# Kernel tuning notes

Hardware: AMD Instinct MI355X
Metric: run time of the kernel (lower is better)

## Reference

```python
import jax, jax.numpy as jnp
import numpy as np

SIZE = 2
STRIDE = 1


def _odd_shapes(input_size, k, size, stride):
    # Mirrors maxpool2d.shape_for_odd_columns. slices=[row_start,row_end,col_start,col_end]
    slices = [None, None, None, None]
    pads = [0, 0, 0, 0]  # (left, right, top, bottom) -- torch ZeroPad2d order
    pads[0] = k
    pads[1] = max(0, k - (input_size[3] - 1) % (2 * stride))
    pads[2] = size - k // 2
    constraint = input_size[2] - 1 - ((input_size[2] - 1 - stride // 2) // stride) * stride
    bottom = size - (k + 1) // 2 - constraint
    if bottom >= 0:
        pads[3] = bottom
    else:
        slices[1] = bottom
    return slices, pads


def _even_shapes(input_size, k, size, stride):
    # Mirrors maxpool2d.shape_for_even_columns
    slices = [None, None, None, None]
    pads = [0, 0, 0, 0]
    left = k - stride
    if left >= 0:
        pads[0] = left
    else:
        slices[2] = -left
    pads[1] = max(0, k - (input_size[3] - 1 - stride) % (2 * stride))
    top_shift = -(k % 2) if stride % 2 == 1 else 0
    top = size - k // 2 + top_shift - stride // 2
    if top >= 0:
        pads[2] = top
    else:
        slices[0] = -top
    bottom_shift = 0 if stride % 2 == 1 else -(k % 2)
    pads[3] = max(0, size - k // 2 + bottom_shift - (input_size[2] - stride // 2 - 1) % stride)
    return slices, pads


def _max_pool2d(x, kernel, stride, dilation):
    # Equivalent of F.max_pool2d with VALID padding + window dilation.
    init = jnp.array(-jnp.inf, x.dtype)
    return jax.lax.reduce_window(
        x, init, jax.lax.max,
        window_dimensions=(1, 1, kernel[0], kernel[1]),
        window_strides=(1, 1, stride[0], stride[1]),
        padding='VALID',
        window_dilation=(1, 1, dilation[0], dilation[1]),
    )


def _branch(x, slices, pads, kernel, stride, dilation):
    s0, s1, s2, s3 = slices
    x = x[:, :, s0:s1, s2:s3]
    # torch ZeroPad2d pads with zeros (data values), so zeros participate in max.
    x = jnp.pad(x, ((0, 0), (0, 0), (pads[2], pads[3]), (pads[0], pads[1])))
    return _max_pool2d(x, kernel, stride, dilation)


def _hex_maxpool(x, size, stride):
    input_size = x.shape  # (B, C, H, W) -- all static under jit
    odd = None
    even = None
    for i in range(size + 1):
        kernel = (1 + 2 * size - i, 1 if i == 0 else 2)
        dilation = (1, 1) if i == 0 else (1, 2 * i)
        pool_stride = (stride, 2 * stride)
        o_sl, o_pd = _odd_shapes(input_size, i, size, stride)
        e_sl, e_pd = _even_shapes(input_size, i, size, stride)
        o = _branch(x, o_sl, o_pd, kernel, pool_stride, dilation)
        e = _branch(x, e_sl, e_pd, kernel, pool_stride, dilation)
        odd = o if odd is None else jnp.maximum(odd, o)
        even = e if even is None else jnp.maximum(even, e)
    cat = jnp.concatenate((odd, even), axis=3)
    n_odd = odd.shape[3]
    n_even = even.shape[3]
    if n_odd == n_even:
        idx = [i + x_ * n_even for i in range(n_even) for x_ in range(2)]
    else:
        idx = [i + x_ * n_odd for i in range(n_even) for x_ in range(2)]
        idx.append(n_even)
    return cat[:, :, :, np.asarray(idx)]


def setup_inputs() -> dict:
    key = jax.random.key(0)
    x = jax.random.normal(key, (16, 64, 256, 256), dtype=jnp.float32)
    return {"input": x}


def reference(input) -> jnp.ndarray:
    return _hex_maxpool(input, SIZE, STRIDE)
```

## Files before the change

kernel.cpp:

```cpp
#include <hip/hip_runtime.h>

#define IMG_H 256
#define IMG_W 256
#define ROWS_PER_WAVE 64
#define STRIPS 4
#define N_IMG 1024

__device__ __forceinline__ float4 fmax4(const float4 a, const float4 b) {
    return make_float4(fmaxf(a.x, b.x), fmaxf(a.y, b.y), fmaxf(a.z, b.z), fmaxf(a.w, b.w));
}

__global__ __launch_bounds__(256) void hex_maxpool_kernel(const float* __restrict__ in,
                                                          float* __restrict__ out) {
    const int lane  = threadIdx.x & 63;
    const int wave  = threadIdx.x >> 6;
    const int gw    = blockIdx.x * 4 + wave;
    const int img   = gw >> 2;
    const int strip = gw & 3;
    const int h0    = strip * ROWS_PER_WAVE;
    const int col   = lane * 4;

    const float* p = in  + (size_t)img * (IMG_H * IMG_W);
    float*       q = out + (size_t)img * (IMG_H * IMG_W);

    auto load_row = [&](int r) -> float4 {
        if ((unsigned)r < (unsigned)IMG_H) {
            return *reinterpret_cast<const float4*>(p + r * IMG_W + col);
        }
        return make_float4(0.f, 0.f, 0.f, 0.f);
    };

    float4 w0 = load_row(h0 - 2);
    float4 w1 = load_row(h0 - 1);
    float4 w2 = load_row(h0);
    float4 w3 = load_row(h0 + 1);
    float4 w4 = load_row(h0 + 2);

    for (int h = h0; h < h0 + ROWS_PER_WAVE; ++h) {
        const float4 wn = load_row(h + 3);

        const float4 m3 = fmax4(fmax4(w1, w2), w3);
        const float4 bu = fmax4(m3, w0);
        const float4 bd = fmax4(m3, w4);
        const float4 a5 = fmax4(bu, w4);

        float Lbuw = __shfl_up(bu.w, 1);
        float Lm3z = __shfl_up(m3.z, 1);
        float Lm3w = __shfl_up(m3.w, 1);
        float Rbdx = __shfl_down(bd.x, 1);
        float Rm3x = __shfl_down(m3.x, 1);
        float Rm3y = __shfl_down(m3.y, 1);
        if (lane == 0)  { Lbuw = 0.f; Lm3z = 0.f; Lm3w = 0.f; }
        if (lane == 63) { Rbdx = 0.f; Rm3x = 0.f; Rm3y = 0.f; }

        float4 o;
        o.x = fmaxf(fmaxf(fmaxf(a5.x, Lbuw), bu.y), fmaxf(Lm3z, m3.z));
        o.y = fmaxf(fmaxf(fmaxf(a5.y, bd.x), bd.z), fmaxf(Lm3w, m3.w));
        o.z = fmaxf(fmaxf(fmaxf(a5.z, bu.y), bu.w), fmaxf(m3.x, Rm3x));
        o.w = fmaxf(fmaxf(fmaxf(a5.w, bd.z), Rbdx), fmaxf(m3.y, Rm3y));

        *reinterpret_cast<float4*>(q + h * IMG_W + col) = o;

        w0 = w1; w1 = w2; w2 = w3; w3 = w4; w4 = wn;
    }
}

extern "C" void kernel_launch(void* const* d_in, const int* in_sizes, int n_in,
                              void* d_out, int out_size, void* d_ws, size_t ws_size,
                              hipStream_t stream) {
    (void)in_sizes; (void)n_in; (void)d_ws; (void)ws_size; (void)out_size;
    const float* in = (const float*)d_in[0];
    float* out = (float*)d_out;
    hex_maxpool_kernel<<<N_IMG * STRIPS / 4, 256, 0, stream>>>(in, out);
}
```

Before: 437.6 us.

## Split images into 16-row strips staged through LDS via direct global-to-LDS loads

```diff
diff --git a/kernel.cpp b/kernel.cpp
--- a/kernel.cpp
+++ b/kernel.cpp
@@ -1,9 +1,11 @@
 #include <hip/hip_runtime.h>
+#include <stdint.h>
 
 #define IMG_H 256
 #define IMG_W 256
-#define ROWS_PER_WAVE 64
-#define STRIPS 4
+#define STRIP_ROWS 16
+#define LDS_ROWS   20
+#define STRIPS_PER_IMG 16
 #define N_IMG 1024
 
 __device__ __forceinline__ float4 fmax4(const float4 a, const float4 b) {
@@ -12,33 +14,36 @@
 
 __global__ __launch_bounds__(256) void hex_maxpool_kernel(const float* __restrict__ in,
                                                           float* __restrict__ out) {
+    __shared__ float smem[LDS_ROWS * IMG_W];
+
     const int lane  = threadIdx.x & 63;
     const int wave  = threadIdx.x >> 6;
-    const int gw    = blockIdx.x * 4 + wave;
-    const int img   = gw >> 2;
-    const int strip = gw & 3;
-    const int h0    = strip * ROWS_PER_WAVE;
-    const int col   = lane * 4;
+    const int img   = blockIdx.x >> 4;
+    const int strip = blockIdx.x & 15;
+    const int S     = strip * STRIP_ROWS;
 
     const float* p = in  + (size_t)img * (IMG_H * IMG_W);
     float*       q = out + (size_t)img * (IMG_H * IMG_W);
 
-    auto load_row = [&](int r) -> float4 {
-        if ((unsigned)r < (unsigned)IMG_H) {
-            return *reinterpret_cast<const float4*>(p + r * IMG_W + col);
+#pragma unroll
+    for (int j5 = 0; j5 < 5; ++j5) {
+        const int j = wave * 5 + j5;
+        const int g = S - 2 + j;
+        if ((unsigned)g < (unsigned)IMG_H) {
+            const float* gp = p + (size_t)g * IMG_W + lane * 4;
+            __builtin_amdgcn_global_load_lds(
+                (const __attribute__((address_space(1))) uint32_t*)gp,
+                (__attribute__((address_space(3))) uint32_t*)&smem[j * IMG_W],
+                16, 0, 0);
+        } else {
+            *reinterpret_cast<float4*>(&smem[j * IMG_W + lane * 4]) =
+                make_float4(0.f, 0.f, 0.f, 0.f);
         }
-        return make_float4(0.f, 0.f, 0.f, 0.f);
-    };
+    }
+    __syncthreads();
 
-    float4 w0 = load_row(h0 - 2);
-    float4 w1 = load_row(h0 - 1);
-    float4 w2 = load_row(h0);
-    float4 w3 = load_row(h0 + 1);
-    float4 w4 = load_row(h0 + 2);
-
-    for (int h = h0; h < h0 + ROWS_PER_WAVE; ++h) {
-        const float4 wn = load_row(h + 3);
-
+    auto hexrow = [&](const float4 w0, const float4 w1, const float4 w2,
+                      const float4 w3, const float4 w4) -> float4 {
         const float4 m3 = fmax4(fmax4(w1, w2), w3);
         const float4 bu = fmax4(m3, w0);
         const float4 bd = fmax4(m3, w4);
@@ -58,10 +63,20 @@
         o.y = fmaxf(fmaxf(fmaxf(a5.y, bd.x), bd.z), fmaxf(Lm3w, m3.w));
         o.z = fmaxf(fmaxf(fmaxf(a5.z, bu.y), bu.w), fmaxf(m3.x, Rm3x));
         o.w = fmaxf(fmaxf(fmaxf(a5.w, bd.z), Rbdx), fmaxf(m3.y, Rm3y));
+        return o;
+    };
 
-        *reinterpret_cast<float4*>(q + h * IMG_W + col) = o;
+    const int base = wave * 4;
+    float4 r[8];
+#pragma unroll
+    for (int j = 0; j < 8; ++j) {
+        r[j] = *reinterpret_cast<const float4*>(&smem[(base + j) * IMG_W + lane * 4]);
+    }
 
-        w0 = w1; w1 = w2; w2 = w3; w3 = w4; w4 = wn;
+#pragma unroll
+    for (int k = 0; k < 4; ++k) {
+        const float4 o = hexrow(r[k], r[k + 1], r[k + 2], r[k + 3], r[k + 4]);
+        *reinterpret_cast<float4*>(q + (size_t)(S + base + k) * IMG_W + lane * 4) = o;
     }
 }
 
@@ -71,5 +86,5 @@
     (void)in_sizes; (void)n_in; (void)d_ws; (void)ws_size; (void)out_size;
     const float* in = (const float*)d_in[0];
     float* out = (float*)d_out;
-    hex_maxpool_kernel<<<N_IMG * STRIPS / 4, 256, 0, stream>>>(in, out);
+    hex_maxpool_kernel<<<N_IMG * STRIPS_PER_IMG, 256, 0, stream>>>(in, out);
 }
```

Measured after the change: 425.6 us. 2.7% less time.

## Assign one output row per wave instead of a rolling 64-row strip

Applied to the files above, without the earlier changes.

```diff
diff --git a/kernel.cpp b/kernel.cpp
--- a/kernel.cpp
+++ b/kernel.cpp
@@ -2,67 +2,58 @@
 
 #define IMG_H 256
 #define IMG_W 256
-#define ROWS_PER_WAVE 64
-#define STRIPS 4
 #define N_IMG 1024
 
 __device__ __forceinline__ float4 fmax4(const float4 a, const float4 b) {
     return make_float4(fmaxf(a.x, b.x), fmaxf(a.y, b.y), fmaxf(a.z, b.z), fmaxf(a.w, b.w));
 }
 
-__global__ __launch_bounds__(256) void hex_maxpool_kernel(const float* __restrict__ in,
-                                                          float* __restrict__ out) {
-    const int lane  = threadIdx.x & 63;
-    const int wave  = threadIdx.x >> 6;
-    const int gw    = blockIdx.x * 4 + wave;
-    const int img   = gw >> 2;
-    const int strip = gw & 3;
-    const int h0    = strip * ROWS_PER_WAVE;
-    const int col   = lane * 4;
+__global__ __launch_bounds__(256, 8) void hex_maxpool_kernel(const float* __restrict__ in,
+                                                             float* __restrict__ out) {
+    const int lane = threadIdx.x & 63;
+    const int wave = threadIdx.x >> 6;
+    const int gw   = blockIdx.x * 4 + wave;
+    const int img  = gw >> 8;
+    const int h    = gw & 255;
+    const int col  = lane * 4;
 
     const float* p = in  + (size_t)img * (IMG_H * IMG_W);
     float*       q = out + (size_t)img * (IMG_H * IMG_W);
 
-    auto load_row = [&](int r) -> float4 {
-        if ((unsigned)r < (unsigned)IMG_H) {
-            return *reinterpret_cast<const float4*>(p + r * IMG_W + col);
-        }
-        return make_float4(0.f, 0.f, 0.f, 0.f);
-    };
+    const int hm2 = h - 2, hm1 = h - 1, hp1 = h + 1, hp2 = h + 2;
+    float4 w0 = *reinterpret_cast<const float4*>(p + (size_t)(hm2 < 0 ? 0 : hm2) * IMG_W + col);
+    float4 w1 = *reinterpret_cast<const float4*>(p + (size_t)(hm1 < 0 ? 0 : hm1) * IMG_W + col);
+    float4 w2 = *reinterpret_cast<const float4*>(p + (size_t)h * IMG_W + col);
+    float4 w3 = *reinterpret_cast<const float4*>(p + (size_t)(hp1 > 255 ? 255 : hp1) * IMG_W + col);
+    float4 w4 = *reinterpret_cast<const float4*>(p + (size_t)(hp2 > 255 ? 255 : hp2) * IMG_W + col);
 
-    float4 w0 = load_row(h0 - 2);
-    float4 w1 = load_row(h0 - 1);
-    float4 w2 = load_row(h0);
-    float4 w3 = load_row(h0 + 1);
-    float4 w4 = load_row(h0 + 2);
+    const float4 z = make_float4(0.f, 0.f, 0.f, 0.f);
+    if (hm2 < 0)   w0 = z;
+    if (hm1 < 0)   w1 = z;
+    if (hp1 > 255) w3 = z;
+    if (hp2 > 255) w4 = z;
 
-    for (int h = h0; h < h0 + ROWS_PER_WAVE; ++h) {
-        const float4 wn = load_row(h + 3);
+    const float4 m3 = fmax4(fmax4(w1, w2), w3);
+    const float4 bu = fmax4(m3, w0);
+    const float4 bd = fmax4(m3, w4);
+    const float4 a5 = fmax4(bu, w4);
 
-        const float4 m3 = fmax4(fmax4(w1, w2), w3);
-        const float4 bu = fmax4(m3, w0);
-        const float4 bd = fmax4(m3, w4);
-        const float4 a5 = fmax4(bu, w4);
+    float Lbuw = __shfl_up(bu.w, 1);
+    float Lm3z = __shfl_up(m3.z, 1);
+    float Lm3w = __shfl_up(m3.w, 1);
+    float Rbdx = __shfl_down(bd.x, 1);
+    float Rm3x = __shfl_down(m3.x, 1);
+    float Rm3y = __shfl_down(m3.y, 1);
+    if (lane == 0)  { Lbuw = 0.f; Lm3z = 0.f; Lm3w = 0.f; }
+    if (lane == 63) { Rbdx = 0.f; Rm3x = 0.f; Rm3y = 0.f; }
 
-        float Lbuw = __shfl_up(bu.w, 1);
-        float Lm3z = __shfl_up(m3.z, 1);
-        float Lm3w = __shfl_up(m3.w, 1);
-        float Rbdx = __shfl_down(bd.x, 1);
-        float Rm3x = __shfl_down(m3.x, 1);
-        float Rm3y = __shfl_down(m3.y, 1);
-        if (lane == 0)  { Lbuw = 0.f; Lm3z = 0.f; Lm3w = 0.f; }
-        if (lane == 63) { Rbdx = 0.f; Rm3x = 0.f; Rm3y = 0.f; }
+    float4 o;
+    o.x = fmaxf(fmaxf(fmaxf(a5.x, Lbuw), bu.y), fmaxf(Lm3z, m3.z));
+    o.y = fmaxf(fmaxf(fmaxf(a5.y, bd.x), bd.z), fmaxf(Lm3w, m3.w));
+    o.z = fmaxf(fmaxf(fmaxf(a5.z, bu.y), bu.w), fmaxf(m3.x, Rm3x));
+    o.w = fmaxf(fmaxf(fmaxf(a5.w, bd.z), Rbdx), fmaxf(m3.y, Rm3y));
 
-        float4 o;
-        o.x = fmaxf(fmaxf(fmaxf(a5.x, Lbuw), bu.y), fmaxf(Lm3z, m3.z));
-        o.y = fmaxf(fmaxf(fmaxf(a5.y, bd.x), bd.z), fmaxf(Lm3w, m3.w));
-        o.z = fmaxf(fmaxf(fmaxf(a5.z, bu.y), bu.w), fmaxf(m3.x, Rm3x));
-        o.w = fmaxf(fmaxf(fmaxf(a5.w, bd.z), Rbdx), fmaxf(m3.y, Rm3y));
-
-        *reinterpret_cast<float4*>(q + h * IMG_W + col) = o;
-
-        w0 = w1; w1 = w2; w2 = w3; w3 = w4; w4 = wn;
-    }
+    *reinterpret_cast<float4*>(q + (size_t)h * IMG_W + col) = o;
 }
 
 extern "C" void kernel_launch(void* const* d_in, const int* in_sizes, int n_in,
@@ -71,5 +62,5 @@
     (void)in_sizes; (void)n_in; (void)d_ws; (void)ws_size; (void)out_size;
     const float* in = (const float*)d_in[0];
     float* out = (float*)d_out;
-    hex_maxpool_kernel<<<N_IMG * STRIPS / 4, 256, 0, stream>>>(in, out);
+    hex_maxpool_kernel<<<N_IMG * IMG_H / 4, 256, 0, stream>>>(in, out);
 }
```

Result: faster. 426.9 us (-2.4%).
